# Performance work log

Measured on AMD Instinct MI355X. Metric: run time of the kernel, lower is better.

Reference implementation:

```python
import jax, jax.numpy as jnp
import numpy as np

B, S, D = 2, 2048, 1024
H, DH = 16, 64
NEG = -1e9


def setup_inputs() -> dict:
    key = jax.random.key(0)
    ks = jax.random.split(key, 4)
    hidden_states = jax.random.normal(ks[0], (B, S, D), dtype=jnp.float32)
    # additive causal mask: 0 where allowed, -1e9 where masked
    causal = jnp.tril(jnp.ones((S, S), dtype=bool))
    attention_mask = jnp.where(causal, 0.0, NEG).astype(jnp.float32)[None, None]
    Wqkv = jax.random.normal(ks[1], (D, 3 * H * DH), dtype=jnp.float32) * (1.0 / np.sqrt(D))
    bqkv = jnp.zeros((3 * H * DH,), dtype=jnp.float32)
    Wproj = jax.random.normal(ks[2], (H * DH, D), dtype=jnp.float32) * (1.0 / np.sqrt(H * DH))
    bproj = jnp.zeros((D,), dtype=jnp.float32)
    return {"hidden_states": hidden_states, "attention_mask": attention_mask,
            "Wqkv": Wqkv, "bqkv": bqkv, "Wproj": Wproj, "bproj": bproj}


def reference(hidden_states, attention_mask, Wqkv, bqkv, Wproj, bproj):
    b, s, _ = hidden_states.shape
    scale = 1.0 / np.sqrt(DH)
    qkv = hidden_states @ Wqkv + bqkv                      # [b, s, 3*H*DH]
    q, k, v = jnp.split(qkv, 3, axis=-1)
    # [b, s, H*DH] -> [b, H, s, DH]
    def split_heads(x):
        return x.reshape(b, s, H, DH).transpose(0, 2, 1, 3)
    q, k, v = split_heads(q), split_heads(k), split_heads(v)
    scores = jnp.einsum('bhqd,bhkd->bhqk', q, k) * scale   # [b, H, s, s]
    scores = scores + attention_mask
    probs = jax.nn.softmax(scores, axis=-1)
    attn = jnp.einsum('bhqk,bhkd->bhqd', probs, v)         # [b, H, s, DH]
    attn = attn.transpose(0, 2, 1, 3).reshape(b, s, H * DH)
    out = attn @ Wproj + bproj                             # [b, s, D]
    return out
```

## Files before the change

### kernel.cpp

```cpp
#include <hip/hip_runtime.h>
#include <stdint.h>

#define B_ 2
#define S_ 2048
#define D_ 1024
#define H_ 16
#define DH_ 64
#define M_ 4096
#define LOG2E 1.44269504088896340736f

typedef __attribute__((ext_vector_type(8))) short short8;
typedef __attribute__((ext_vector_type(4))) float f32x4;
typedef __attribute__((ext_vector_type(16))) float f32x16;

__device__ __forceinline__ unsigned short f2bf(float f) {
  union { float f; uint32_t u; } x; x.f = f;
  uint32_t u = x.u;
  u += 0x7FFFu + ((u >> 16) & 1u);
  return (unsigned short)(u >> 16);
}

__device__ __forceinline__ unsigned int pack_bf(float lo, float hi2) {
  return (unsigned int)f2bf(lo) | ((unsigned int)f2bf(hi2) << 16);
}

__device__ __forceinline__ void gll16(const void* g, void* l) {
  __builtin_amdgcn_global_load_lds(
      (__attribute__((address_space(1))) void*)(g),
      (__attribute__((address_space(3))) void*)(l), 16, 0, 0);
}

__global__ __launch_bounds__(256) void k_prep(const float* __restrict__ hs,
                                              const float* __restrict__ Wqkv,
                                              const float* __restrict__ Wproj,
                                              unsigned short* __restrict__ hid,
                                              unsigned short* __restrict__ wqkvT,
                                              unsigned short* __restrict__ wprT) {
  __shared__ unsigned short tile[32][33];
  const int id = blockIdx.x;
  if (id < 4096) {
    const int i = id * 256 + threadIdx.x;
    float4 v = reinterpret_cast<const float4*>(hs)[i];
    ushort4 o;
    o.x = f2bf(v.x); o.y = f2bf(v.y); o.z = f2bf(v.z); o.w = f2bf(v.w);
    reinterpret_cast<ushort4*>(hid)[i] = o;
    return;
  }
  const float* W;
  unsigned short* WT;
  int N, i;
  if (id < 7168) { i = id - 4096; W = Wqkv; WT = wqkvT; N = 3072; }
  else           { i = id - 7168; W = Wproj; WT = wprT; N = 1024; }
  const int nb = (N == 3072) ? 96 : 32;
  const int n0 = (i % nb) * 32, k0 = (i / nb) * 32;
  const int tx = threadIdx.x & 31, ty = threadIdx.x >> 5;
#pragma unroll
  for (int j = 0; j < 4; j++) {
    int k = ty + j * 8;
    tile[k][tx] = f2bf(W[(long)(k0 + k) * N + n0 + tx]);
  }
  __syncthreads();
#pragma unroll
  for (int j = 0; j < 4; j++) {
    int n = ty + j * 8;
    WT[(long)(n0 + n) * 1024 + k0 + tx] = tile[tx][n];
  }
}

template <int MODE, int BN>
__global__ __launch_bounds__(256) void k_gemm(
    const unsigned short* __restrict__ A,
    const unsigned short* __restrict__ BT,
    const float* __restrict__ bias,
    void* __restrict__ out0,
    unsigned short* __restrict__ outk,
    unsigned short* __restrict__ outv,
    int M, int N, int K) {
  constexpr int JN = BN / 32;
  __shared__ __align__(16) unsigned short lds_a[128 * 32];
  __shared__ __align__(16) unsigned short lds_b[BN * 32];
  const int t = threadIdx.x;
  const int w = t >> 6, l = t & 63;
  const int g = l >> 4, x = l & 15;
  const int wr = w >> 1, wc = w & 1;
  const long m0 = (long)blockIdx.x * 128, n0 = (long)blockIdx.y * BN;

  f32x4 acc[4][JN];
#pragma unroll
  for (int i = 0; i < 4; i++)
#pragma unroll
    for (int j = 0; j < JN; j++) acc[i][j] = (f32x4){0.f, 0.f, 0.f, 0.f};

  const unsigned short* ga = A + (m0 + 16 * w + (l >> 2)) * (long)K + (l & 3) * 8;
  const unsigned short* gb = BT + (n0 + 16 * w + (l >> 2)) * (long)K + (l & 3) * 8;
  unsigned short* la = lds_a + w * 512;
  unsigned short* lb = lds_b + w * 512;

  for (int k0 = 0; k0 < K; k0 += 32) {
    __syncthreads();
    gll16(ga + k0, la);
    gll16(ga + k0 + 64 * (long)K, la + 2048);
    gll16(gb + k0, lb);
    if (BN == 128) gll16(gb + k0 + 64 * (long)K, lb + 2048);
    __syncthreads();
    short8 af[4], bfr[JN];
#pragma unroll
    for (int i = 0; i < 4; i++)
      af[i] = *reinterpret_cast<const short8*>(lds_a + (wr * 64 + i * 16 + x) * 32 + g * 8);
#pragma unroll
    for (int j = 0; j < JN; j++)
      bfr[j] = *reinterpret_cast<const short8*>(
          lds_b + (wc * (BN / 2) + j * 16 + x) * 32 + g * 8);
#pragma unroll
    for (int i = 0; i < 4; i++)
#pragma unroll
      for (int j = 0; j < JN; j++)
        acc[i][j] = __builtin_amdgcn_mfma_f32_16x16x32_bf16(af[i], bfr[j], acc[i][j], 0, 0, 0);
  }

#pragma unroll
  for (int i = 0; i < 4; i++) {
#pragma unroll
    for (int j = 0; j < JN; j++) {
#pragma unroll
      for (int r = 0; r < 4; r++) {
        const long m = m0 + wr * 64 + i * 16 + 4 * g + r;
        const long n = n0 + wc * (BN / 2) + j * 16 + x;
        float v = acc[i][j][r] + bias[n];
        if (MODE == 1) {
          ((float*)out0)[m * N + n] = v;
        } else {
          const int b = (int)(m >> 11), s = (int)(m & 2047);
          const int which = (int)(n >> 10);
          const int rem = (int)(n & 1023);
          const int h = rem >> 6, d = rem & 63;
          const long idx = (((long)(b * H_ + h)) * S_ + s) * DH_ + d;
          unsigned short bv = f2bf(v);
          if (which == 0) ((unsigned short*)out0)[idx] = bv;
          else if (which == 1) outk[idx] = bv;
          else outv[idx] = bv;
        }
      }
    }
  }
}

__global__ __launch_bounds__(256) void k_tr_v(const unsigned short* __restrict__ v,
                                              unsigned short* __restrict__ vt) {
  __shared__ __align__(16) unsigned short tile[64][72];
  const int bh = blockIdx.y;
  const int s0 = blockIdx.x * 64;
  const int t = threadIdx.x;
  const int r = t >> 2;
  const int c = (t & 3) * 16;
  const unsigned short* src = v + ((long)bh * S_ + s0 + r) * DH_ + c;
  *reinterpret_cast<short8*>(&tile[r][c]) = *reinterpret_cast<const short8*>(src);
  *reinterpret_cast<short8*>(&tile[r][c + 8]) = *reinterpret_cast<const short8*>(src + 8);
  __syncthreads();
  unsigned short* dst = vt + ((long)bh * DH_ + r) * S_ + s0 + c;
#pragma unroll
  for (int jj = 0; jj < 2; jj++) {
    short8 o;
#pragma unroll
    for (int j = 0; j < 8; j++) o[j] = (short)tile[c + jj * 8 + j][r];
    *reinterpret_cast<short8*>(dst + jj * 8) = o;
  }
}

__global__ __launch_bounds__(256, 1) void k_attn(const unsigned short* __restrict__ qb_,
                                                 const unsigned short* __restrict__ kb,
                                                 const unsigned short* __restrict__ vt,
                                                 unsigned short* __restrict__ attn_out) {
  __shared__ __align__(16) unsigned short lds_k[2][4096];
  __shared__ __align__(16) unsigned short lds_v[2][4096];

  const int t0 = threadIdx.x;
  const int w = t0 >> 6, l = t0 & 63;
  const int q32 = l & 31, hi = l >> 5;
  const int r7 = q32 & 7;
  const int lr = l >> 3, sch = (l & 7) ^ lr;

  const int id = blockIdx.x;
  const int xcd = id & 7, slot = id >> 3;
  const int bh = xcd + 8 * (slot >> 4);
  const int craw = slot & 15;
  const int qc = (slot & 32) ? craw : (15 - craw);

  const int b = bh >> 4, h = bh & 15;
  const long kvbase = (long)bh * S_ * DH_;
  const long vtbase = (long)bh * DH_ * S_;
  const float SC = 0.125f * LOG2E;

  const int q0p = qc * 128;
  const int q0w = q0p + 32 * w;
  const int qg = q0w + q32;
  const int nt = 2 * qc + 2;

  short8 qf[4];
#pragma unroll
  for (int f = 0; f < 4; f++)
    qf[f] = *reinterpret_cast<const short8*>(qb_ + kvbase + (long)qg * DH_ + 16 * f + 8 * hi);

#pragma unroll
  for (int i = 0; i < 2; i++) {
    gll16(kb + kvbase + (long)(16 * w + 8 * i + lr) * DH_ + sch * 8,
          &lds_k[0][w * 1024 + i * 512]);
    gll16(vt + vtbase + (long)(16 * w + 8 * i + lr) * S_ + sch * 8,
          &lds_v[0][w * 1024 + i * 512]);
  }

  f32x16 oacc[2];
#pragma unroll
  for (int dt = 0; dt < 2; dt++)
#pragma unroll
    for (int r = 0; r < 16; r++) oacc[dt][r] = 0.f;
  float m = -1.0e30f, lown = 0.f;

  asm volatile("s_waitcnt vmcnt(0)" ::: "memory");
  __syncthreads();

  for (int tt = 0; tt < nt; tt++) {
    const int kv0 = tt * 64;
    if (tt + 1 < nt) {
      const int nb = (tt + 1) & 1;
      const int kvn = kv0 + 64;
#pragma unroll
      for (int i = 0; i < 2; i++) {
        gll16(kb + kvbase + (long)(kvn + 16 * w + 8 * i + lr) * DH_ + sch * 8,
              &lds_k[nb][w * 1024 + i * 512]);
        gll16(vt + vtbase + (long)(16 * w + 8 * i + lr) * S_ + kvn + sch * 8,
              &lds_v[nb][w * 1024 + i * 512]);
      }
    }

    if (kv0 <= q0w + 31) {
      const unsigned short* lk = lds_k[tt & 1];
      const unsigned short* lv = lds_v[tt & 1];

      f32x16 sa[2];
#pragma unroll
      for (int ks = 0; ks < 2; ks++) {
#pragma unroll
        for (int r = 0; r < 16; r++) sa[ks][r] = 0.f;
#pragma unroll
        for (int f = 0; f < 4; f++) {
          short8 kf = *reinterpret_cast<const short8*>(
              lk + (32 * ks + q32) * 64 + (((2 * f + hi) ^ r7) << 3));
          sa[ks] = __builtin_amdgcn_mfma_f32_32x32x16_bf16(kf, qf[f], sa[ks], 0, 0, 0);
        }
      }

      float p[32];
#pragma unroll
      for (int ks = 0; ks < 2; ks++)
#pragma unroll
        for (int r = 0; r < 16; r++) p[16 * ks + r] = sa[ks][r] * SC;

      const bool diag = (kv0 + 63 > q0w);
      if (diag) {
#pragma unroll
        for (int ks = 0; ks < 2; ks++)
#pragma unroll
          for (int r = 0; r < 16; r++) {
            const int kvg = kv0 + 32 * ks + (r & 3) + 8 * (r >> 2) + 4 * hi;
            if (kvg > qg) p[16 * ks + r] = -1.0e30f;
          }
      }

      float mx[16];
#pragma unroll
      for (int r = 0; r < 16; r++) mx[r] = fmaxf(p[r], p[r + 16]);
#pragma unroll
      for (int st = 8; st >= 1; st >>= 1)
#pragma unroll
        for (int r = 0; r < 8; r++)
          if (r < st) mx[r] = fmaxf(mx[r], mx[r + st]);
      float pmax = fmaxf(mx[0], __shfl_xor(mx[0], 32, 64));

      if (__any(pmax > m + 8.0f)) {
        const float mn = fmaxf(m, pmax);
        const float fsc = exp2f(m - mn);
        m = mn;
        lown *= fsc;
#pragma unroll
        for (int r = 0; r < 16; r++) {
          const int rr = (r & 3) + 8 * (r >> 2) + 4 * hi;
          const float fr = __int_as_float(
              __builtin_amdgcn_ds_bpermute(rr << 2, __float_as_int(fsc)));
          oacc[0][r] *= fr;
          oacc[1][r] *= fr;
        }
      }

#pragma unroll
      for (int i = 0; i < 32; i++) p[i] = exp2f(p[i] - m);

      float sm[16];
#pragma unroll
      for (int r = 0; r < 16; r++) sm[r] = p[r] + p[r + 16];
#pragma unroll
      for (int st = 8; st >= 1; st >>= 1)
#pragma unroll
        for (int r = 0; r < 8; r++)
          if (r < st) sm[r] += sm[r + st];
      lown += sm[0];

#pragma unroll
      for (int s4 = 0; s4 < 4; s4++) {
        const int bse = 8 * s4;
        unsigned int t0p = pack_bf(p[bse + 0], p[bse + 1]);
        unsigned int t1p = pack_bf(p[bse + 2], p[bse + 3]);
        unsigned int t2p = pack_bf(p[bse + 4], p[bse + 5]);
        unsigned int t3p = pack_bf(p[bse + 6], p[bse + 7]);
        unsigned int t0x = __shfl_xor(t0p, 32, 64);
        unsigned int t1x = __shfl_xor(t1p, 32, 64);
        unsigned int t2x = __shfl_xor(t2p, 32, 64);
        unsigned int t3x = __shfl_xor(t3p, 32, 64);
        union { unsigned int u[4]; short8 s8; } pa;
        pa.u[0] = hi ? t2x : t0p;
        pa.u[1] = hi ? t3x : t1p;
        pa.u[2] = hi ? t2p : t0x;
        pa.u[3] = hi ? t3p : t1x;
#pragma unroll
        for (int dt = 0; dt < 2; dt++) {
          short8 vf = *reinterpret_cast<const short8*>(
              lv + (32 * dt + q32) * 64 + (((2 * s4 + hi) ^ r7) << 3));
          oacc[dt] = __builtin_amdgcn_mfma_f32_32x32x16_bf16(pa.s8, vf, oacc[dt], 0, 0, 0);
        }
      }
    }

    asm volatile("s_waitcnt vmcnt(0)" ::: "memory");
    __syncthreads();
  }

  const float lt = lown + __shfl_xor(lown, 32, 64);
  const float linv = 1.0f / lt;
#pragma unroll
  for (int r = 0; r < 16; r++) {
    const int rr = (r & 3) + 8 * (r >> 2) + 4 * hi;
    const float li = __int_as_float(
        __builtin_amdgcn_ds_bpermute(rr << 2, __float_as_int(linv)));
    const long row = (long)b * S_ + q0w + rr;
#pragma unroll
    for (int dt = 0; dt < 2; dt++)
      attn_out[row * (H_ * DH_) + h * DH_ + 32 * dt + q32] = f2bf(oacc[dt][r] * li);
  }
}

extern "C" void kernel_launch(void* const* d_in, const int* in_sizes, int n_in,
                              void* d_out, int out_size, void* d_ws, size_t ws_size,
                              hipStream_t stream) {
  (void)in_sizes; (void)n_in; (void)out_size; (void)ws_size;
  const float* hs    = (const float*)d_in[0];
  const float* Wqkv  = (const float*)d_in[2];
  const float* bqkv  = (const float*)d_in[3];
  const float* Wproj = (const float*)d_in[4];
  const float* bproj = (const float*)d_in[5];
  float* out = (float*)d_out;

  unsigned short* ws    = (unsigned short*)d_ws;
  unsigned short* hid   = ws;
  unsigned short* wqkvT = hid + 4194304;
  unsigned short* wprT  = wqkvT + 3145728;
  unsigned short* q_b   = wprT + 1048576;
  unsigned short* k_b   = q_b + 4194304;
  unsigned short* v_b   = k_b + 4194304;
  unsigned short* vt_b  = v_b + 4194304;
  unsigned short* ao    = vt_b + 4194304;

  k_prep<<<8192, 256, 0, stream>>>(hs, Wqkv, Wproj, hid, wqkvT, wprT);
  k_gemm<0, 128><<<dim3(32, 24), 256, 0, stream>>>(hid, wqkvT, bqkv, (void*)q_b, k_b, v_b,
                                                   4096, 3072, 1024);
  k_tr_v<<<dim3(32, 32), 256, 0, stream>>>(v_b, vt_b);
  k_attn<<<512, 256, 0, stream>>>(q_b, k_b, vt_b, ao);
  k_gemm<1, 64><<<dim3(32, 16), 256, 0, stream>>>(ao, wprT, bproj, (void*)out, nullptr, nullptr,
                                                  4096, 1024, 1024);
}
```

Measured before the change: 224.7 us.

## Split long causal attention rows along KV and merge partials in a combine kernel

Query chunks with longer causal ranges are split into up to four KV segments. Each segment runs as its own block and writes an unnormalized bf16 partial output plus its running max and sum. A new combine kernel rescales the partials and normalizes them into the attention output. This is meant to balance work across blocks and raise the block count from 512 to 1280. The cost is an extra launch, roughly 32 MB of partial-output traffic, an added bf16 rounding before the final normalization, and the loss of the earlier XCD-aware block ordering.

New measurement: 228.1 us. About the same (+1.5%).

```diff
diff --git a/kernel.cpp b/kernel.cpp
--- a/kernel.cpp
+++ b/kernel.cpp
@@ -18,6 +18,10 @@
   uint32_t u = x.u;
   u += 0x7FFFu + ((u >> 16) & 1u);
   return (unsigned short)(u >> 16);
+}
+
+__device__ __forceinline__ float bf2f(unsigned short u) {
+  union { uint32_t u; float f; } x; x.u = (uint32_t)u << 16; return x.f;
 }
 
 __device__ __forceinline__ unsigned int pack_bf(float lo, float hi2) {
@@ -170,31 +174,40 @@
 __global__ __launch_bounds__(256, 1) void k_attn(const unsigned short* __restrict__ qb_,
                                                  const unsigned short* __restrict__ kb,
                                                  const unsigned short* __restrict__ vt,
-                                                 unsigned short* __restrict__ attn_out) {
+                                                 unsigned short* __restrict__ po,
+                                                 float* __restrict__ pm,
+                                                 float* __restrict__ pl) {
   __shared__ __align__(16) unsigned short lds_k[2][4096];
   __shared__ __align__(16) unsigned short lds_v[2][4096];
 
-  const int t0 = threadIdx.x;
-  const int w = t0 >> 6, l = t0 & 63;
+  const int t0_ = threadIdx.x;
+  const int w = t0_ >> 6, l = t0_ & 63;
   const int q32 = l & 31, hi = l >> 5;
   const int r7 = q32 & 7;
   const int lr = l >> 3, sch = (l & 7) ^ lr;
-
-  const int id = blockIdx.x;
-  const int xcd = id & 7, slot = id >> 3;
-  const int bh = xcd + 8 * (slot >> 4);
-  const int craw = slot & 15;
-  const int qc = (slot & 32) ? craw : (15 - craw);
-
-  const int b = bh >> 4, h = bh & 15;
+  const int bh = blockIdx.y;
   const long kvbase = (long)bh * S_ * DH_;
   const long vtbase = (long)bh * DH_ * S_;
   const float SC = 0.125f * LOG2E;
 
+  int qc = 0, sp = 0;
+  {
+    int sx = blockIdx.x, acc = 0;
+    for (int q = 0; q < 16; q++) {
+      const int ns = (q >> 2) + 1;
+      if (sx < acc + ns) { qc = q; sp = sx - acc; break; }
+      acc += ns;
+    }
+  }
+  const int nspl = (qc >> 2) + 1;
+  const int nt = 2 * qc + 2;
+  const int ts = sp * nt / nspl;
+  const int te = (sp + 1) * nt / nspl;
+
   const int q0p = qc * 128;
   const int q0w = q0p + 32 * w;
   const int qg = q0w + q32;
-  const int nt = 2 * qc + 2;
+  const long pidx = ((long)(bh * 16 + qc)) * 4 + sp;
 
   short8 qf[4];
 #pragma unroll
@@ -203,9 +216,9 @@
 
 #pragma unroll
   for (int i = 0; i < 2; i++) {
-    gll16(kb + kvbase + (long)(16 * w + 8 * i + lr) * DH_ + sch * 8,
+    gll16(kb + kvbase + (long)(ts * 64 + 16 * w + 8 * i + lr) * DH_ + sch * 8,
           &lds_k[0][w * 1024 + i * 512]);
-    gll16(vt + vtbase + (long)(16 * w + 8 * i + lr) * S_ + sch * 8,
+    gll16(vt + vtbase + (long)(16 * w + 8 * i + lr) * S_ + ts * 64 + sch * 8,
           &lds_v[0][w * 1024 + i * 512]);
   }
 
@@ -219,10 +232,10 @@
   asm volatile("s_waitcnt vmcnt(0)" ::: "memory");
   __syncthreads();
 
-  for (int tt = 0; tt < nt; tt++) {
+  for (int tt = ts; tt < te; tt++) {
     const int kv0 = tt * 64;
-    if (tt + 1 < nt) {
-      const int nb = (tt + 1) & 1;
+    if (tt + 1 < te) {
+      const int nb = (tt + 1 - ts) & 1;
       const int kvn = kv0 + 64;
 #pragma unroll
       for (int i = 0; i < 2; i++) {
@@ -234,8 +247,8 @@
     }
 
     if (kv0 <= q0w + 31) {
-      const unsigned short* lk = lds_k[tt & 1];
-      const unsigned short* lv = lds_v[tt & 1];
+      const unsigned short* lk = lds_k[(tt - ts) & 1];
+      const unsigned short* lv = lds_v[(tt - ts) & 1];
 
       f32x16 sa[2];
 #pragma unroll
@@ -335,16 +348,74 @@
   }
 
   const float lt = lown + __shfl_xor(lown, 32, 64);
-  const float linv = 1.0f / lt;
+  if (hi == 0) {
+    pm[pidx * 128 + 32 * w + q32] = m;
+    pl[pidx * 128 + 32 * w + q32] = lt;
+  }
+  unsigned short* pob = po + pidx * 8192;
 #pragma unroll
   for (int r = 0; r < 16; r++) {
     const int rr = (r & 3) + 8 * (r >> 2) + 4 * hi;
-    const float li = __int_as_float(
-        __builtin_amdgcn_ds_bpermute(rr << 2, __float_as_int(linv)));
-    const long row = (long)b * S_ + q0w + rr;
+    const int row = 32 * w + rr;
 #pragma unroll
     for (int dt = 0; dt < 2; dt++)
-      attn_out[row * (H_ * DH_) + h * DH_ + 32 * dt + q32] = f2bf(oacc[dt][r] * li);
+      pob[row * 64 + 32 * dt + q32] = f2bf(oacc[dt][r]);
+  }
+}
+
+__global__ __launch_bounds__(256) void k_comb(const unsigned short* __restrict__ po,
+                                              const float* __restrict__ pm,
+                                              const float* __restrict__ pl,
+                                              unsigned short* __restrict__ ao) {
+  const int qc = blockIdx.x, bh = blockIdx.y;
+  const int b = bh >> 4, h = bh & 15;
+  const int nspl = (qc >> 2) + 1;
+  const int t = threadIdx.x;
+  const int r = t >> 1, c0 = (t & 1) * 32;
+  const long pbase = ((long)(bh * 16 + qc)) * 4;
+
+  float mi[4], li[4], wi[4];
+  float ms = -3.0e38f;
+#pragma unroll
+  for (int i = 0; i < 4; i++) {
+    if (i < nspl) {
+      mi[i] = pm[(pbase + i) * 128 + r];
+      li[i] = pl[(pbase + i) * 128 + r];
+      ms = fmaxf(ms, mi[i]);
+    }
+  }
+  float wsum = 0.f;
+#pragma unroll
+  for (int i = 0; i < 4; i++) {
+    if (i < nspl) {
+      wi[i] = exp2f(mi[i] - ms);
+      wsum += wi[i] * li[i];
+    }
+  }
+  float acc[32];
+#pragma unroll
+  for (int j = 0; j < 32; j++) acc[j] = 0.f;
+#pragma unroll
+  for (int i = 0; i < 4; i++) {
+    if (i < nspl) {
+      const unsigned short* src = po + (pbase + i) * 8192 + r * 64 + c0;
+#pragma unroll
+      for (int v = 0; v < 4; v++) {
+        short8 s = *reinterpret_cast<const short8*>(src + v * 8);
+#pragma unroll
+        for (int j = 0; j < 8; j++)
+          acc[v * 8 + j] += wi[i] * bf2f((unsigned short)s[j]);
+      }
+    }
+  }
+  const float inv = 1.0f / wsum;
+  unsigned short* dst = ao + ((long)b * S_ + qc * 128 + r) * (H_ * DH_) + h * DH_ + c0;
+#pragma unroll
+  for (int v = 0; v < 4; v++) {
+    short8 o;
+#pragma unroll
+    for (int j = 0; j < 8; j++) o[j] = (short)f2bf(acc[v * 8 + j] * inv);
+    *reinterpret_cast<short8*>(dst + v * 8) = o;
   }
 }
 
@@ -368,12 +439,16 @@
   unsigned short* v_b   = k_b + 4194304;
   unsigned short* vt_b  = v_b + 4194304;
   unsigned short* ao    = vt_b + 4194304;
+  unsigned short* po    = ao + 4194304;
+  float* pm = (float*)(po + 16777216);
+  float* pl = pm + 262144;
 
   k_prep<<<8192, 256, 0, stream>>>(hs, Wqkv, Wproj, hid, wqkvT, wprT);
   k_gemm<0, 128><<<dim3(32, 24), 256, 0, stream>>>(hid, wqkvT, bqkv, (void*)q_b, k_b, v_b,
                                                    4096, 3072, 1024);
   k_tr_v<<<dim3(32, 32), 256, 0, stream>>>(v_b, vt_b);
-  k_attn<<<512, 256, 0, stream>>>(q_b, k_b, vt_b, ao);
+  k_attn<<<dim3(40, 32), 256, 0, stream>>>(q_b, k_b, vt_b, po, pm, pl);
+  k_comb<<<dim3(16, 32), 256, 0, stream>>>(po, pm, pl, ao);
   k_gemm<1, 64><<<dim3(32, 16), 256, 0, stream>>>(ao, wprT, bproj, (void*)out, nullptr, nullptr,
                                                   4096, 1024, 1024);
 }
```
